# Optimization experiments

Hardware: AMD Instinct MI355X
Metric: run time of the kernel (lower is better)

The kernel has to match this reference:

```python
import jax, jax.numpy as jnp
import numpy as np

N = 100000   # nodes
E = 1600000  # edges per meta-path graph
D_IN = 256
H = 4        # num_heads
F = 32       # out_feats per head
D_HID = H * F  # 128
D_SEM = 128  # semantic attention hidden dim
C = 8        # output classes
NEG_SLOPE = 0.2


def setup_inputs() -> dict:
    key = jax.random.key(0)
    ks = jax.random.split(key, 24)
    inp = {
        "x": jax.random.normal(ks[0], (N, D_IN), dtype=jnp.float32),
        "src0": jax.random.randint(ks[1], (E,), 0, N),
        "dst0": jax.random.randint(ks[2], (E,), 0, N),
        "ew0": jax.random.uniform(ks[3], (E,), dtype=jnp.float32),
        "src1": jax.random.randint(ks[4], (E,), 0, N),
        "dst1": jax.random.randint(ks[5], (E,), 0, N),
        "ew1": jax.random.uniform(ks[6], (E,), dtype=jnp.float32),
    }
    s_in = 1.0 / np.sqrt(D_IN)
    s_f = 1.0 / np.sqrt(F)
    s_h = 1.0 / np.sqrt(D_HID)
    s_s = 1.0 / np.sqrt(D_SEM)
    # GAT params for meta-path 0 and 1 (tuple feat -> separate fc_src/fc_dst)
    inp["Wsrc0"] = jax.random.normal(ks[7], (D_IN, D_HID), dtype=jnp.float32) * s_in
    inp["Wdst0"] = jax.random.normal(ks[8], (D_IN, D_HID), dtype=jnp.float32) * s_in
    inp["al0"] = jax.random.normal(ks[9], (H, F), dtype=jnp.float32) * s_f
    inp["ar0"] = jax.random.normal(ks[10], (H, F), dtype=jnp.float32) * s_f
    inp["b0"] = jnp.zeros((D_HID,), dtype=jnp.float32)
    inp["Wsrc1"] = jax.random.normal(ks[11], (D_IN, D_HID), dtype=jnp.float32) * s_in
    inp["Wdst1"] = jax.random.normal(ks[12], (D_IN, D_HID), dtype=jnp.float32) * s_in
    inp["al1"] = jax.random.normal(ks[13], (H, F), dtype=jnp.float32) * s_f
    inp["ar1"] = jax.random.normal(ks[14], (H, F), dtype=jnp.float32) * s_f
    inp["b1"] = jnp.zeros((D_HID,), dtype=jnp.float32)
    # Semantic attention: Linear(D_HID->128) -> tanh -> Linear(128->1, no bias)
    inp["Wp1"] = jax.random.normal(ks[15], (D_HID, D_SEM), dtype=jnp.float32) * s_h
    inp["bp1"] = jnp.zeros((D_SEM,), dtype=jnp.float32)
    inp["Wp2"] = jax.random.normal(ks[16], (D_SEM, 1), dtype=jnp.float32) * s_s
    # Prediction head
    inp["Wo"] = jax.random.normal(ks[17], (D_HID, C), dtype=jnp.float32) * s_h
    inp["bo"] = jnp.zeros((C,), dtype=jnp.float32)
    return inp


def gat_conv(x, Wsrc, Wdst, al, ar, b, src, dst, ew):
    # feat_src/feat_dst: [N, H, F]
    fs = (x @ Wsrc).reshape(N, H, F)
    fd = (x @ Wdst).reshape(N, H, F)
    el = jnp.einsum('nhf,hf->nh', fs, al)  # [N, H]
    er = jnp.einsum('nhf,hf->nh', fd, ar)  # [N, H]
    e = jax.nn.leaky_relu(el[src] + er[dst], negative_slope=NEG_SLOPE)  # [E, H]
    a = jax.nn.sigmoid(e) * ew[:, None]  # [E, H]  (sigmoid attention * edge_weight)
    m = fs[src] * a[:, :, None]  # [E, H, F]
    out = jax.ops.segment_sum(m, dst, num_segments=N)  # [N, H, F]
    out = out + b.reshape(1, H, F)
    return jax.nn.elu(out).reshape(N, H * F)


def semantic_attention(z, Wp1, bp1, Wp2):
    # z: [N, P, D_HID]
    w = jnp.tanh(z @ Wp1 + bp1) @ Wp2  # [N, P, 1]
    w = w.mean(axis=0)                  # [P, 1]
    beta = jax.nn.softmax(w, axis=0)    # softmax over meta-paths
    return (beta[None] * z).sum(axis=1)  # [N, D_HID]


def reference(x, src0, dst0, ew0, src1, dst1, ew1,
              Wsrc0, Wdst0, al0, ar0, b0,
              Wsrc1, Wdst1, al1, ar1, b1,
              Wp1, bp1, Wp2, Wo, bo):
    z0 = gat_conv(x, Wsrc0, Wdst0, al0, ar0, b0, src0, dst0, ew0)
    z1 = gat_conv(x, Wsrc1, Wdst1, al1, ar1, b1, src1, dst1, ew1)
    z = jnp.stack([z0, z1], axis=1)  # [N, 2, H*F]
    h = semantic_attention(z, Wp1, bp1, Wp2)  # [N, H*F]
    return h @ Wo + bo  # [N, C]
```

## Files before the change

### kernel.cpp

```cpp
#include <hip/hip_runtime.h>
#include <hip/hip_fp16.h>
#include <math.h>

#define N_NODES 100000
#define N_EDGES 1600000
#define D_IN    256
#define D_HID   128
#define NH      4
#define NF      32
#define D_SEM   128
#define NC      8
#define NEG_SLOPE 0.2f
#define BUCKET  64
#define BIN_SHIFT 9
#define BINS    196
#define BIN_CAP 9216
#define CHUNK   8192

typedef _Float16 half8 __attribute__((ext_vector_type(8)));
typedef float    floatx4 __attribute__((ext_vector_type(4)));

struct BinArgs {
    const int*   src[2];
    const int*   dst[2];
    const float* ew[2];
    int*         gcur[2];
    uint2*       binned[2];
};
struct BucketArgs {
    const int*   gcur[2];
    const uint2* binned[2];
    int*         cnt[2];
    unsigned*    edg[2];
};

__global__ __launch_bounds__(256) void prep(const float* __restrict__ Ws0,
                                            const float* __restrict__ Ws1,
                                            const float* __restrict__ Wd0,
                                            const float* __restrict__ ar0,
                                            const float* __restrict__ Wd1,
                                            const float* __restrict__ ar1,
                                            const float* __restrict__ Wp1,
                                            __half* __restrict__ WTA,
                                            __half* __restrict__ WP1T) {
    int g = blockIdx.x * 256 + threadIdx.x;
    if (g < 32768) {
        int col = g >> 8, k = g & 255;
        WTA[(size_t)col*256 + k] = __float2half_rn(Ws0[k*D_HID + col]);
    } else if (g < 65536) {
        int g2 = g - 32768;
        int col = g2 >> 8, k = g2 & 255;
        WTA[(size_t)(128 + col)*256 + k] = __float2half_rn(Ws1[k*D_HID + col]);
    } else if (g < 73728) {
        int g2 = g - 65536;
        int j = g2 >> 8, k = g2 & 255;
        int p = j >> 4, hh = j & 15;
        float s = 0.f;
        if (hh < 4) {
            const float* Wd = p ? Wd1 : Wd0;
            const float* ar = p ? ar1 : ar0;
            for (int f = 0; f < NF; ++f)
                s = fmaf(Wd[k*D_HID + hh*NF + f], ar[hh*NF + f], s);
        }
        WTA[(size_t)(256 + j)*256 + k] = __float2half_rn(s);
    } else if (g < 90112) {
        int g2 = g - 73728;
        int c = g2 >> 7, k = g2 & 127;
        WP1T[g2] = __float2half_rn(Wp1[k*D_SEM + c]);
    }
}

__global__ __launch_bounds__(256, 4) void fs_half(const float* __restrict__ x,
                                                  const __half* __restrict__ WTA,
                                                  const float* __restrict__ al0,
                                                  const float* __restrict__ al1,
                                                  __half* __restrict__ FS0,
                                                  __half* __restrict__ FS1,
                                                  float* __restrict__ eler) {
    __shared__ unsigned short xs[64][256];
    __shared__ unsigned short wsB[144][64];
    int tid = threadIdx.x;
    int row0 = blockIdx.x * 64;
    int P = blockIdx.y;
    __half* FSP = P ? FS1 : FS0;
    int wid = tid >> 6, lane = tid & 63;
    int lr = lane & 15, lk = lane >> 4;

    #pragma unroll
    for (int i = 0; i < 8; ++i) {
        int id = tid + i*256;
        int r = id >> 5, c8 = (id & 31) << 3;
        int grow = row0 + r;
        float4 v0 = make_float4(0.f,0.f,0.f,0.f), v1 = v0;
        if (grow < N_NODES) {
            v0 = *(const float4*)&x[(size_t)grow*D_IN + c8];
            v1 = *(const float4*)&x[(size_t)grow*D_IN + c8 + 4];
        }
        __half2 h0 = __floats2half2_rn(v0.x, v0.y);
        __half2 h1 = __floats2half2_rn(v0.z, v0.w);
        __half2 h2 = __floats2half2_rn(v1.x, v1.y);
        __half2 h3 = __floats2half2_rn(v1.z, v1.w);
        uint4 pk;
        pk.x = *(unsigned*)&h0; pk.y = *(unsigned*)&h1;
        pk.z = *(unsigned*)&h2; pk.w = *(unsigned*)&h3;
        int ch = c8 >> 3;
        *(uint4*)&xs[r][((ch ^ (r & 7)) << 3)] = pk;
    }

    floatx4 acc[4][2];
    floatx4 acc4[4];
    #pragma unroll
    for (int m = 0; m < 4; ++m) {
        acc4[m] = (floatx4){0.f, 0.f, 0.f, 0.f};
        #pragma unroll
        for (int n = 0; n < 2; ++n) acc[m][n] = (floatx4){0.f, 0.f, 0.f, 0.f};
    }
    __syncthreads();

    for (int kc = 0; kc < 4; ++kc) {
        #pragma unroll
        for (int i = 0; i < 9; ++i) {
            int id = tid + i*256;
            int cl = id >> 4, c4 = (id & 15) << 2;
            int gcol = (cl < 128) ? (P*128 + cl) : (256 + P*16 + (cl - 128));
            uint2 pk = *(const uint2*)&WTA[(size_t)gcol*256 + kc*64 + c4];
            int cc = (((c4 >> 3) ^ (cl & 7)) << 3) + (c4 & 7);
            *(uint2*)&wsB[cl][cc] = pk;
        }
        __syncthreads();
        #pragma unroll
        for (int kk = 0; kk < 2; ++kk) {
            int kl = kk*4 + lk;
            int kg = kc*8 + kl;
            half8 a[4], b[2], b4;
            #pragma unroll
            for (int n = 0; n < 2; ++n) {
                int cl = wid*32 + n*16 + lr;
                b[n] = *(half8*)&wsB[cl][((kl ^ (cl & 7)) << 3)];
            }
            if (wid == 0) {
                int cl = 128 + lr;
                b4 = *(half8*)&wsB[cl][((kl ^ (cl & 7)) << 3)];
            }
            #pragma unroll
            for (int m = 0; m < 4; ++m) {
                int r = m*16 + lr;
                a[m] = *(half8*)&xs[r][((kg ^ (r & 7)) << 3)];
            }
            #pragma unroll
            for (int m = 0; m < 4; ++m)
                #pragma unroll
                for (int n = 0; n < 2; ++n)
                    acc[m][n] = __builtin_amdgcn_mfma_f32_16x16x32_f16(a[m], b[n], acc[m][n], 0, 0, 0);
            if (wid == 0) {
                #pragma unroll
                for (int m = 0; m < 4; ++m)
                    acc4[m] = __builtin_amdgcn_mfma_f32_16x16x32_f16(a[m], b4, acc4[m], 0, 0, 0);
            }
        }
        __syncthreads();
    }

    {
        const float* al = P ? al1 : al0;
        float av0 = al[wid*NF + lr];
        float av1 = al[wid*NF + 16 + lr];
        #pragma unroll
        for (int m = 0; m < 4; ++m)
            #pragma unroll
            for (int r4 = 0; r4 < 4; ++r4) {
                float s0 = acc[m][0][r4]*av0 + acc[m][1][r4]*av1;
                #pragma unroll
                for (int o = 1; o < 16; o <<= 1) s0 += __shfl_xor(s0, o);
                int row = row0 + m*16 + lk*4 + r4;
                if (lr == 0 && row < N_NODES)
                    eler[(P*2)*400000 + row*4 + wid] = s0;
            }
    }
    if (wid == 0 && lr < 4) {
        #pragma unroll
        for (int m = 0; m < 4; ++m)
            #pragma unroll
            for (int r4 = 0; r4 < 4; ++r4) {
                int row = row0 + m*16 + lk*4 + r4;
                if (row < N_NODES)
                    eler[(P*2+1)*400000 + row*4 + lr] = acc4[m][r4];
            }
    }

    __syncthreads();
    unsigned short* cstage = &xs[0][0];
    #pragma unroll
    for (int n = 0; n < 2; ++n) {
        int cl = wid*32 + n*16 + lr;
        #pragma unroll
        for (int m = 0; m < 4; ++m)
            #pragma unroll
            for (int r4 = 0; r4 < 4; ++r4) {
                int rr = m*16 + lk*4 + r4;
                __half hv = __float2half_rn(acc[m][n][r4]);
                cstage[rr*128 + cl] = *(unsigned short*)&hv;
            }
    }
    __syncthreads();
    #pragma unroll
    for (int i = 0; i < 4; ++i) {
        int id = tid + i*256;
        int r = id >> 4, c8 = (id & 15) << 3;
        int grow = row0 + r;
        if (grow < N_NODES)
            *(uint4*)&FSP[(size_t)grow*D_HID + c8] = *(uint4*)&cstage[r*128 + c8];
    }
}

__global__ __launch_bounds__(1024) void bin_kernel(BinArgs A) {
    __shared__ uint2 stage[CHUNK];
    __shared__ unsigned char binof[CHUNK];
    __shared__ int bcnt[256], boff[256], gbase[256], brun[256];
    int P = blockIdx.y;
    const int*   src = A.src[P];
    const int*   dst = A.dst[P];
    const float* ew  = A.ew[P];
    int*         gcur = A.gcur[P];
    uint2*       binned = A.binned[P];

    int tid = threadIdx.x;
    int c0 = blockIdx.x * CHUNK;
    int C = N_EDGES - c0; if (C > CHUNK) C = CHUNK;
    if (C <= 0) return;

    if (tid < 256) bcnt[tid] = 0;
    __syncthreads();
    for (int j = tid; j < C; j += 1024)
        atomicAdd(&bcnt[dst[c0 + j] >> BIN_SHIFT], 1);
    __syncthreads();

    int v = (tid < 256) ? bcnt[tid] : 0;
    if (tid < 256) boff[tid] = v;
    __syncthreads();
    for (int o = 1; o < 256; o <<= 1) {
        int u = (tid < 256 && tid >= o) ? boff[tid - o] : 0;
        __syncthreads();
        if (tid < 256) boff[tid] += u;
        __syncthreads();
    }
    if (tid < 256) {
        boff[tid] -= v;
        brun[tid] = 0;
        if (tid < BINS) gbase[tid] = v ? atomicAdd(&gcur[tid], v) : 0;
    }
    __syncthreads();

    for (int j = tid; j < C; j += 1024) {
        int e = c0 + j;
        int d = dst[e];
        int b = d >> BIN_SHIFT;
        unsigned q = (unsigned)(ew[e] * 32767.f + 0.5f);
        int p = atomicAdd(&brun[b], 1);
        int sl = boff[b] + p;
        stage[sl] = make_uint2(((unsigned)src[e] << 15) | q, (unsigned)d);
        binof[sl] = (unsigned char)b;
    }
    __syncthreads();

    for (int j = tid; j < C; j += 1024) {
        int b = binof[j];
        int off = gbase[b] + (j - boff[b]);
        if (off < BIN_CAP) binned[b * BIN_CAP + off] = stage[j];
    }
}

__global__ __launch_bounds__(1024) void bucket_kernel(BucketArgs A) {
    __shared__ unsigned buck[256 * BUCKET];
    __shared__ int lcnt[256];
    int P = blockIdx.y;
    const int*   gcur   = A.gcur[P];
    const uint2* binned = A.binned[P];
    int*         cnt    = A.cnt[P];
    unsigned*    edg    = A.edg[P];

    int tid = threadIdx.x;
    int nb = blockIdx.x;
    int b  = nb >> 1;
    int n0 = nb << 8;
    int lo = (nb & 1) << 8;
    if (tid < 256) lcnt[tid] = 0;
    __syncthreads();

    int cE = gcur[b]; if (cE > BIN_CAP) cE = BIN_CAP;
    int bn0 = b << BIN_SHIFT;
    for (int j = tid; j < cE; j += 1024) {
        uint2 r = binned[b * BIN_CAP + j];
        int w = ((int)r.y - bn0) - lo;
        if ((unsigned)w < 256u) {
            int p = atomicAdd(&lcnt[w], 1);
            if (p < BUCKET) buck[(w << 6) + p] = r.x;
        }
    }
    __syncthreads();

    const uint4* b4 = (const uint4*)buck;
    uint4* e4 = (uint4*)edg;
    for (int i = tid; i < 256 * BUCKET / 4; i += 1024) {
        int node = n0 + (i >> 4);
        int used = lcnt[i >> 4];
        if (node < N_NODES && ((i & 15) << 2) < used)
            e4[((size_t)node << 4) + (i & 15)] = b4[i];
    }
    if (tid < 256) {
        int node = n0 + tid;
        if (node < N_NODES) cnt[node] = lcnt[tid] < BUCKET ? lcnt[tid] : BUCKET;
    }
}

__global__ __launch_bounds__(256) void agg_kernel(const __half* __restrict__ FS,
                                                  const float* __restrict__ el,
                                                  const float* __restrict__ er,
                                                  const int* __restrict__ cnt,
                                                  const unsigned* __restrict__ edg,
                                                  const float* __restrict__ bias,
                                                  __half* __restrict__ zh) {
    int wv = (blockIdx.x * 256 + threadIdx.x) >> 6;
    int lane = threadIdx.x & 63;
    if (wv >= N_NODES) return;
    int q  = lane >> 4;
    int ql = lane & 15;
    int hh = lane & 3;
    float erh = er[wv*4 + hh];
    int cn = cnt[wv];
    if (cn > BUCKET) cn = BUCKET;
    int beg = wv << 6;
    const __half* fsq = FS + (ql << 3);

    float4 a0 = make_float4(0.f,0.f,0.f,0.f);
    float4 a1 = make_float4(0.f,0.f,0.f,0.f);

    int nIt = (cn + 15) >> 4;
    for (int it = 0; it < nIt; ++it) {
        int jb = it << 4;
        int sl = jb + (lane >> 2);
        int slc = sl < cn ? sl : cn - 1;
        unsigned w = edg[beg + slc];
        int s = (int)(w >> 15);
        float a = (float)(w & 32767u) * (1.f / 32767.f);
        float v = el[s*4 + hh] + erh;
        v = v > 0.f ? v : NEG_SLOPE * v;
        a = a * __builtin_amdgcn_rcpf(1.f + __expf(-v));
        a = sl < cn ? a : 0.f;
        #pragma unroll
        for (int u = 0; u < 4; ++u) {
            int e = (u << 2) + q;
            int su = jb + e;
            int ssrc = __shfl(s, e << 2);
            uint4 raw = make_uint4(0u, 0u, 0u, 0u);
            if (su < cn) raw = *(const uint4*)&fsq[(size_t)ssrc * D_HID];
            float av = __shfl(a, (e << 2) | (ql >> 2));
            float2 f0 = __half22float2(*(__half2*)&raw.x);
            float2 f1 = __half22float2(*(__half2*)&raw.y);
            float2 f2 = __half22float2(*(__half2*)&raw.z);
            float2 f3 = __half22float2(*(__half2*)&raw.w);
            a0.x = fmaf(f0.x, av, a0.x); a0.y = fmaf(f0.y, av, a0.y);
            a0.z = fmaf(f1.x, av, a0.z); a0.w = fmaf(f1.y, av, a0.w);
            a1.x = fmaf(f2.x, av, a1.x); a1.y = fmaf(f2.y, av, a1.y);
            a1.z = fmaf(f3.x, av, a1.z); a1.w = fmaf(f3.y, av, a1.w);
        }
    }

    #pragma unroll
    for (int o = 16; o < 64; o <<= 1) {
        a0.x += __shfl_xor(a0.x, o); a0.y += __shfl_xor(a0.y, o);
        a0.z += __shfl_xor(a0.z, o); a0.w += __shfl_xor(a0.w, o);
        a1.x += __shfl_xor(a1.x, o); a1.y += __shfl_xor(a1.y, o);
        a1.z += __shfl_xor(a1.z, o); a1.w += __shfl_xor(a1.w, o);
    }

    if (q < 2) {
        int c = (ql << 3) + (q << 2);
        float4 r = q ? a1 : a0;
        float4 bv = *(const float4*)&bias[c];
        r.x += bv.x; r.y += bv.y; r.z += bv.z; r.w += bv.w;
        r.x = r.x > 0.f ? r.x : expm1f(r.x);
        r.y = r.y > 0.f ? r.y : expm1f(r.y);
        r.z = r.z > 0.f ? r.z : expm1f(r.z);
        r.w = r.w > 0.f ? r.w : expm1f(r.w);
        __half2 h0 = __floats2half2_rn(r.x, r.y);
        __half2 h1 = __floats2half2_rn(r.z, r.w);
        uint2 pk; pk.x = *(unsigned*)&h0; pk.y = *(unsigned*)&h1;
        *(uint2*)&zh[(size_t)wv*D_HID + c] = pk;
    }
}

__global__ __launch_bounds__(256) void sem_mfma(const __half* __restrict__ zh0,
                                                const __half* __restrict__ zh1,
                                                const __half* __restrict__ WP1T,
                                                const float* __restrict__ bp1,
                                                const float* __restrict__ Wp2,
                                                float* __restrict__ wsum) {
    __shared__ unsigned short zs[64][128];
    __shared__ unsigned short ps[128][128];
    __shared__ float red[4];
    const __half* z = blockIdx.y ? zh1 : zh0;
    int tid = threadIdx.x;
    int row0 = blockIdx.x * 64;
    int wid = tid >> 6, lane = tid & 63;
    int wm = wid >> 1, wn = wid & 1;
    int lr = lane & 15, lk = lane >> 4;

    #pragma unroll
    for (int i = 0; i < 4; ++i) {
        int id = tid + i*256;
        int r = id >> 4, ch = id & 15;
        int grow = row0 + r;
        uint4 pk = make_uint4(0u, 0u, 0u, 0u);
        if (grow < N_NODES) pk = *(const uint4*)&z[(size_t)grow*D_HID + (ch << 3)];
        *(uint4*)&zs[r][((ch ^ (r & 7)) << 3)] = pk;
    }
    #pragma unroll
    for (int i = 0; i < 16; ++i) {
        int id = tid + i*256;
        int c = id >> 5, k4 = (id & 31) << 2;
        uint2 pk = *(const uint2*)&WP1T[c*128 + k4];
        int cc = (((k4 >> 3) ^ (c & 7)) << 3) + (k4 & 7);
        *(uint2*)&ps[c][cc] = pk;
    }
    __syncthreads();

    floatx4 acc[2][4];
    #pragma unroll
    for (int m = 0; m < 2; ++m)
        #pragma unroll
        for (int n = 0; n < 4; ++n) acc[m][n] = (floatx4){0.f, 0.f, 0.f, 0.f};

    #pragma unroll
    for (int kk = 0; kk < 4; ++kk) {
        int ksub = kk*4 + lk;
        half8 a[2], b[4];
        #pragma unroll
        for (int m = 0; m < 2; ++m) {
            int r = wm*32 + m*16 + lr;
            a[m] = *(half8*)&zs[r][((ksub ^ (r & 7)) << 3)];
        }
        #pragma unroll
        for (int n = 0; n < 4; ++n) {
            int c = wn*64 + n*16 + lr;
            b[n] = *(half8*)&ps[c][((ksub ^ (c & 7)) << 3)];
        }
        #pragma unroll
        for (int m = 0; m < 2; ++m)
            #pragma unroll
            for (int n = 0; n < 4; ++n)
                acc[m][n] = __builtin_amdgcn_mfma_f32_16x16x32_f16(a[m], b[n], acc[m][n], 0, 0, 0);
    }

    float s = 0.f;
    #pragma unroll
    for (int m = 0; m < 2; ++m)
        #pragma unroll
        for (int n = 0; n < 4; ++n) {
            int col = wn*64 + n*16 + lr;
            float bp = bp1[col];
            float w2 = Wp2[col];
            #pragma unroll
            for (int r4 = 0; r4 < 4; ++r4) {
                int grow = row0 + wm*32 + m*16 + lk*4 + r4;
                if (grow < N_NODES) {
                    float v = acc[m][n][r4] + bp;
                    float t = 1.f - 2.f / (__expf(2.f*v) + 1.f);
                    s = fmaf(t, w2, s);
                }
            }
        }
    #pragma unroll
    for (int o = 1; o < 64; o <<= 1) s += __shfl_xor(s, o);
    if (lane == 0) red[wid] = s;
    __syncthreads();
    if (tid == 0) atomicAdd(&wsum[blockIdx.y], red[0] + red[1] + red[2] + red[3]);
}

__global__ __launch_bounds__(256) void final_kernel(const __half* __restrict__ zh0,
                                                    const __half* __restrict__ zh1,
                                                    const float* __restrict__ Wo,
                                                    const float* __restrict__ bo,
                                                    const float* __restrict__ wsum,
                                                    float* __restrict__ out) {
    __shared__ float z0s[32][132];
    __shared__ float z1s[32][132];
    __shared__ float wos[128*8];
    __shared__ float bos[8];
    int tid = threadIdx.x;
    int n0 = blockIdx.x * 32;
    #pragma unroll
    for (int i = 0; i < 4; ++i) wos[tid + i*256] = Wo[tid + i*256];
    if (tid < 8) bos[tid] = bo[tid];
    #pragma unroll
    for (int i = 0; i < 2; ++i) {
        int id = tid + i*256;
        int r = id >> 4, c8 = (id & 15) << 3;
        uint4 p0 = *(const uint4*)&zh0[(size_t)(n0 + r)*D_HID + c8];
        uint4 p1 = *(const uint4*)&zh1[(size_t)(n0 + r)*D_HID + c8];
        float2 q0 = __half22float2(*(__half2*)&p0.x);
        float2 q1 = __half22float2(*(__half2*)&p0.y);
        float2 q2 = __half22float2(*(__half2*)&p0.z);
        float2 q3 = __half22float2(*(__half2*)&p0.w);
        *(float4*)&z0s[r][c8]     = make_float4(q0.x, q0.y, q1.x, q1.y);
        *(float4*)&z0s[r][c8 + 4] = make_float4(q2.x, q2.y, q3.x, q3.y);
        q0 = __half22float2(*(__half2*)&p1.x);
        q1 = __half22float2(*(__half2*)&p1.y);
        q2 = __half22float2(*(__half2*)&p1.z);
        q3 = __half22float2(*(__half2*)&p1.w);
        *(float4*)&z1s[r][c8]     = make_float4(q0.x, q0.y, q1.x, q1.y);
        *(float4*)&z1s[r][c8 + 4] = make_float4(q2.x, q2.y, q3.x, q3.y);
    }
    __syncthreads();

    float w0 = wsum[0] * (1.f / N_NODES), w1 = wsum[1] * (1.f / N_NODES);
    float m = fmaxf(w0, w1);
    float e0 = __expf(w0 - m), e1 = __expf(w1 - m);
    float b0 = e0 / (e0 + e1), b1 = 1.f - b0;

    int node = tid >> 3, c = tid & 7;
    float s = bos[c];
    #pragma unroll 8
    for (int k = 0; k < 128; ++k) {
        float hk = b0 * z0s[node][k] + b1 * z1s[node][k];
        s = fmaf(hk, wos[k*8 + c], s);
    }
    out[(n0 + node)*NC + c] = s;
}

extern "C" void kernel_launch(void* const* d_in, const int* in_sizes, int n_in,
                              void* d_out, int out_size, void* d_ws, size_t ws_size,
                              hipStream_t stream) {
    const float* x     = (const float*)d_in[0];
    const int*   src0  = (const int*)  d_in[1];
    const int*   dst0  = (const int*)  d_in[2];
    const float* ew0   = (const float*)d_in[3];
    const int*   src1  = (const int*)  d_in[4];
    const int*   dst1  = (const int*)  d_in[5];
    const float* ew1   = (const float*)d_in[6];
    const float* Wsrc0 = (const float*)d_in[7];
    const float* Wdst0 = (const float*)d_in[8];
    const float* al0   = (const float*)d_in[9];
    const float* ar0   = (const float*)d_in[10];
    const float* b0    = (const float*)d_in[11];
    const float* Wsrc1 = (const float*)d_in[12];
    const float* Wdst1 = (const float*)d_in[13];
    const float* al1   = (const float*)d_in[14];
    const float* ar1   = (const float*)d_in[15];
    const float* b1    = (const float*)d_in[16];
    const float* Wp1   = (const float*)d_in[17];
    const float* bp1   = (const float*)d_in[18];
    const float* Wp2   = (const float*)d_in[19];
    const float* Wo    = (const float*)d_in[20];
    const float* bo    = (const float*)d_in[21];
    float* out = (float*)d_out;

    float*    ws     = (float*)d_ws;
    __half*   FS0    = (__half*)ws;
    __half*   FS1    = (__half*)(ws + 6400000);
    __half*   ZH0    = (__half*)(ws + 12800000);
    __half*   ZH1    = (__half*)(ws + 19200000);
    float*    ELER   = ws + 25600000;
    float*    WSUM   = ELER + 1600000;
    __half*   WTA    = (__half*)(WSUM + 8);
    __half*   WP1T   = (__half*)((float*)WTA + 36864);
    int*      CNT0   = (int*)((float*)WP1T + 8192);
    int*      CNT1   = CNT0  + 100000;
    int*      GCUR0  = CNT1  + 100000;
    int*      GCUR1  = GCUR0 + 256;
    unsigned* EDG0   = (unsigned*)(GCUR1 + 256);
    uint2*    BINNED0= (uint2*)(EDG0 + 6400000);
    float*    endser = (float*)BINNED0 + 2*(size_t)BINS*BIN_CAP;
    unsigned* EDG1   = (unsigned*)endser;
    uint2*    BINNED1= (uint2*)(EDG1 + 6400000);
    size_t fused_bytes = (size_t)((float*)BINNED1 + 2*(size_t)BINS*BIN_CAP - ws) * 4;
    bool fused = ws_size >= fused_bytes;
    if (!fused) { EDG1 = EDG0; BINNED1 = BINNED0; }

    hipMemsetAsync(GCUR0, 0, sizeof(int)*512, stream);
    hipMemsetAsync(WSUM, 0, sizeof(float)*4, stream);

    prep<<<352, 256, 0, stream>>>(Wsrc0, Wsrc1, Wdst0, ar0, Wdst1, ar1, Wp1, WTA, WP1T);
    dim3 fsgrid((N_NODES + 63)/64, 2);
    fs_half<<<fsgrid, 256, 0, stream>>>(x, WTA, al0, al1, FS0, FS1, ELER);

    int nchunks = (N_EDGES + CHUNK - 1) / CHUNK;
    if (fused) {
        BinArgs ba = {{src0, src1}, {dst0, dst1}, {ew0, ew1},
                      {GCUR0, GCUR1}, {BINNED0, BINNED1}};
        bin_kernel<<<dim3(nchunks, 2), 1024, 0, stream>>>(ba);
        BucketArgs ka = {{GCUR0, GCUR1}, {BINNED0, BINNED1},
                         {CNT0, CNT1}, {EDG0, EDG1}};
        bucket_kernel<<<dim3(2*BINS, 2), 1024, 0, stream>>>(ka);
        agg_kernel<<<(N_NODES*64)/256, 256, 0, stream>>>(FS0, ELER, ELER + 400000, CNT0, EDG0, b0, ZH0);
        agg_kernel<<<(N_NODES*64)/256, 256, 0, stream>>>(FS1, ELER + 800000, ELER + 1200000, CNT1, EDG1, b1, ZH1);
    } else {
        BinArgs ba0 = {{src0, src0}, {dst0, dst0}, {ew0, ew0},
                       {GCUR0, GCUR0}, {BINNED0, BINNED0}};
        BucketArgs ka0 = {{GCUR0, GCUR0}, {BINNED0, BINNED0},
                          {CNT0, CNT0}, {EDG0, EDG0}};
        bin_kernel<<<dim3(nchunks, 1), 1024, 0, stream>>>(ba0);
        bucket_kernel<<<dim3(2*BINS, 1), 1024, 0, stream>>>(ka0);
        agg_kernel<<<(N_NODES*64)/256, 256, 0, stream>>>(FS0, ELER, ELER + 400000, CNT0, EDG0, b0, ZH0);
        BinArgs ba1 = {{src1, src1}, {dst1, dst1}, {ew1, ew1},
                       {GCUR1, GCUR1}, {BINNED0, BINNED0}};
        BucketArgs ka1 = {{GCUR1, GCUR1}, {BINNED0, BINNED0},
                          {CNT1, CNT1}, {EDG0, EDG0}};
        bin_kernel<<<dim3(nchunks, 1), 1024, 0, stream>>>(ba1);
        bucket_kernel<<<dim3(2*BINS, 1), 1024, 0, stream>>>(ka1);
        agg_kernel<<<(N_NODES*64)/256, 256, 0, stream>>>(FS1, ELER + 800000, ELER + 1200000, CNT1, EDG0, b1, ZH1);
    }

    dim3 semgrid((N_NODES + 63)/64, 2);
    sem_mfma<<<semgrid, 256, 0, stream>>>(ZH0, ZH1, WP1T, bp1, Wp2, WSUM);
    final_kernel<<<N_NODES/32, 256, 0, stream>>>(ZH0, ZH1, Wo, bo, WSUM, out);
}
```

Baseline: 521.5 us.

## Fuse bucketing and GAT aggregation into one kernel using LDS-resident edge buckets

Merges the bucket and aggregation kernels so each 1024-thread block builds per-node edge buckets in shared memory and immediately aggregates them, with each wave handling 16 nodes in sequence. This removes the global EDG/CNT round trip and two kernel launches. In exchange, occupancy drops because of the 64KB LDS per block, and each wave now processes nodes serially, which may expose gather latency. Only 784 blocks run the aggregation instead of the previous large grid.

```diff
diff --git a/kernel.cpp b/kernel.cpp
--- a/kernel.cpp
+++ b/kernel.cpp
@@ -27,11 +27,14 @@
     int*         gcur[2];
     uint2*       binned[2];
 };
-struct BucketArgs {
-    const int*   gcur[2];
-    const uint2* binned[2];
-    int*         cnt[2];
-    unsigned*    edg[2];
+struct BAArgs {
+    const int*    gcur[2];
+    const uint2*  binned[2];
+    const __half* fs[2];
+    const float*  el[2];
+    const float*  er[2];
+    const float*  bias[2];
+    __half*       zh[2];
 };
 
 __global__ __launch_bounds__(256) void prep(const float* __restrict__ Ws0,
@@ -270,14 +273,17 @@
     }
 }
 
-__global__ __launch_bounds__(1024) void bucket_kernel(BucketArgs A) {
+__global__ __launch_bounds__(1024) void bucket_agg(BAArgs A) {
     __shared__ unsigned buck[256 * BUCKET];
     __shared__ int lcnt[256];
     int P = blockIdx.y;
-    const int*   gcur   = A.gcur[P];
-    const uint2* binned = A.binned[P];
-    int*         cnt    = A.cnt[P];
-    unsigned*    edg    = A.edg[P];
+    const int*    gcur   = A.gcur[P];
+    const uint2*  binned = A.binned[P];
+    const __half* FS     = A.fs[P];
+    const float*  el     = A.el[P];
+    const float*  er     = A.er[P];
+    const float*  bias   = A.bias[P];
+    __half*       zh     = A.zh[P];
 
     int tid = threadIdx.x;
     int nb = blockIdx.x;
@@ -299,94 +305,77 @@
     }
     __syncthreads();
 
-    const uint4* b4 = (const uint4*)buck;
-    uint4* e4 = (uint4*)edg;
-    for (int i = tid; i < 256 * BUCKET / 4; i += 1024) {
-        int node = n0 + (i >> 4);
-        int used = lcnt[i >> 4];
-        if (node < N_NODES && ((i & 15) << 2) < used)
-            e4[((size_t)node << 4) + (i & 15)] = b4[i];
-    }
-    if (tid < 256) {
-        int node = n0 + tid;
-        if (node < N_NODES) cnt[node] = lcnt[tid] < BUCKET ? lcnt[tid] : BUCKET;
-    }
-}
-
-__global__ __launch_bounds__(256) void agg_kernel(const __half* __restrict__ FS,
-                                                  const float* __restrict__ el,
-                                                  const float* __restrict__ er,
-                                                  const int* __restrict__ cnt,
-                                                  const unsigned* __restrict__ edg,
-                                                  const float* __restrict__ bias,
-                                                  __half* __restrict__ zh) {
-    int wv = (blockIdx.x * 256 + threadIdx.x) >> 6;
-    int lane = threadIdx.x & 63;
-    if (wv >= N_NODES) return;
+    int wvid = tid >> 6, lane = tid & 63;
     int q  = lane >> 4;
     int ql = lane & 15;
     int hh = lane & 3;
-    float erh = er[wv*4 + hh];
-    int cn = cnt[wv];
-    if (cn > BUCKET) cn = BUCKET;
-    int beg = wv << 6;
     const __half* fsq = FS + (ql << 3);
 
-    float4 a0 = make_float4(0.f,0.f,0.f,0.f);
-    float4 a1 = make_float4(0.f,0.f,0.f,0.f);
-
-    int nIt = (cn + 15) >> 4;
-    for (int it = 0; it < nIt; ++it) {
-        int jb = it << 4;
-        int sl = jb + (lane >> 2);
-        int slc = sl < cn ? sl : cn - 1;
-        unsigned w = edg[beg + slc];
-        int s = (int)(w >> 15);
-        float a = (float)(w & 32767u) * (1.f / 32767.f);
-        float v = el[s*4 + hh] + erh;
-        v = v > 0.f ? v : NEG_SLOPE * v;
-        a = a * __builtin_amdgcn_rcpf(1.f + __expf(-v));
-        a = sl < cn ? a : 0.f;
-        #pragma unroll
-        for (int u = 0; u < 4; ++u) {
-            int e = (u << 2) + q;
-            int su = jb + e;
-            int ssrc = __shfl(s, e << 2);
-            uint4 raw = make_uint4(0u, 0u, 0u, 0u);
-            if (su < cn) raw = *(const uint4*)&fsq[(size_t)ssrc * D_HID];
-            float av = __shfl(a, (e << 2) | (ql >> 2));
-            float2 f0 = __half22float2(*(__half2*)&raw.x);
-            float2 f1 = __half22float2(*(__half2*)&raw.y);
-            float2 f2 = __half22float2(*(__half2*)&raw.z);
-            float2 f3 = __half22float2(*(__half2*)&raw.w);
-            a0.x = fmaf(f0.x, av, a0.x); a0.y = fmaf(f0.y, av, a0.y);
-            a0.z = fmaf(f1.x, av, a0.z); a0.w = fmaf(f1.y, av, a0.w);
-            a1.x = fmaf(f2.x, av, a1.x); a1.y = fmaf(f2.y, av, a1.y);
-            a1.z = fmaf(f3.x, av, a1.z); a1.w = fmaf(f3.y, av, a1.w);
-        }
-    }
-
-    #pragma unroll
-    for (int o = 16; o < 64; o <<= 1) {
-        a0.x += __shfl_xor(a0.x, o); a0.y += __shfl_xor(a0.y, o);
-        a0.z += __shfl_xor(a0.z, o); a0.w += __shfl_xor(a0.w, o);
-        a1.x += __shfl_xor(a1.x, o); a1.y += __shfl_xor(a1.y, o);
-        a1.z += __shfl_xor(a1.z, o); a1.w += __shfl_xor(a1.w, o);
-    }
-
-    if (q < 2) {
-        int c = (ql << 3) + (q << 2);
-        float4 r = q ? a1 : a0;
-        float4 bv = *(const float4*)&bias[c];
-        r.x += bv.x; r.y += bv.y; r.z += bv.z; r.w += bv.w;
-        r.x = r.x > 0.f ? r.x : expm1f(r.x);
-        r.y = r.y > 0.f ? r.y : expm1f(r.y);
-        r.z = r.z > 0.f ? r.z : expm1f(r.z);
-        r.w = r.w > 0.f ? r.w : expm1f(r.w);
-        __half2 h0 = __floats2half2_rn(r.x, r.y);
-        __half2 h1 = __floats2half2_rn(r.z, r.w);
-        uint2 pk; pk.x = *(unsigned*)&h0; pk.y = *(unsigned*)&h1;
-        *(uint2*)&zh[(size_t)wv*D_HID + c] = pk;
+    for (int t = 0; t < 16; ++t) {
+        int nl = wvid*16 + t;
+        int node = n0 + nl;
+        if (node >= N_NODES) break;
+        int cn = lcnt[nl];
+        if (cn > BUCKET) cn = BUCKET;
+        float erh = er[node*4 + hh];
+        unsigned* bk = &buck[nl << 6];
+
+        float4 a0 = make_float4(0.f,0.f,0.f,0.f);
+        float4 a1 = make_float4(0.f,0.f,0.f,0.f);
+
+        int nIt = (cn + 15) >> 4;
+        for (int it = 0; it < nIt; ++it) {
+            int jb = it << 4;
+            int sl = jb + (lane >> 2);
+            int slc = sl < cn ? sl : cn - 1;
+            unsigned w = bk[slc];
+            int s = (int)(w >> 15);
+            float a = (float)(w & 32767u) * (1.f / 32767.f);
+            float v = el[s*4 + hh] + erh;
+            v = v > 0.f ? v : NEG_SLOPE * v;
+            a = a * __builtin_amdgcn_rcpf(1.f + __expf(-v));
+            a = sl < cn ? a : 0.f;
+            #pragma unroll
+            for (int u = 0; u < 4; ++u) {
+                int e = (u << 2) + q;
+                int su = jb + e;
+                int ssrc = __shfl(s, e << 2);
+                uint4 raw = make_uint4(0u, 0u, 0u, 0u);
+                if (su < cn) raw = *(const uint4*)&fsq[(size_t)ssrc * D_HID];
+                float av = __shfl(a, (e << 2) | (ql >> 2));
+                float2 f0 = __half22float2(*(__half2*)&raw.x);
+                float2 f1 = __half22float2(*(__half2*)&raw.y);
+                float2 f2 = __half22float2(*(__half2*)&raw.z);
+                float2 f3 = __half22float2(*(__half2*)&raw.w);
+                a0.x = fmaf(f0.x, av, a0.x); a0.y = fmaf(f0.y, av, a0.y);
+                a0.z = fmaf(f1.x, av, a0.z); a0.w = fmaf(f1.y, av, a0.w);
+                a1.x = fmaf(f2.x, av, a1.x); a1.y = fmaf(f2.y, av, a1.y);
+                a1.z = fmaf(f3.x, av, a1.z); a1.w = fmaf(f3.y, av, a1.w);
+            }
+        }
+
+        #pragma unroll
+        for (int o = 16; o < 64; o <<= 1) {
+            a0.x += __shfl_xor(a0.x, o); a0.y += __shfl_xor(a0.y, o);
+            a0.z += __shfl_xor(a0.z, o); a0.w += __shfl_xor(a0.w, o);
+            a1.x += __shfl_xor(a1.x, o); a1.y += __shfl_xor(a1.y, o);
+            a1.z += __shfl_xor(a1.z, o); a1.w += __shfl_xor(a1.w, o);
+        }
+
+        if (q < 2) {
+            int c = (ql << 3) + (q << 2);
+            float4 r = q ? a1 : a0;
+            float4 bv = *(const float4*)&bias[c];
+            r.x += bv.x; r.y += bv.y; r.z += bv.z; r.w += bv.w;
+            r.x = r.x > 0.f ? r.x : expm1f(r.x);
+            r.y = r.y > 0.f ? r.y : expm1f(r.y);
+            r.z = r.z > 0.f ? r.z : expm1f(r.z);
+            r.w = r.w > 0.f ? r.w : expm1f(r.w);
+            __half2 h0 = __floats2half2_rn(r.x, r.y);
+            __half2 h1 = __floats2half2_rn(r.z, r.w);
+            uint2 pk; pk.x = *(unsigned*)&h0; pk.y = *(unsigned*)&h1;
+            *(uint2*)&zh[(size_t)node*D_HID + c] = pk;
+        }
     }
 }
 
@@ -564,18 +553,14 @@
     float*    WSUM   = ELER + 1600000;
     __half*   WTA    = (__half*)(WSUM + 8);
     __half*   WP1T   = (__half*)((float*)WTA + 36864);
-    int*      CNT0   = (int*)((float*)WP1T + 8192);
-    int*      CNT1   = CNT0  + 100000;
-    int*      GCUR0  = CNT1  + 100000;
+    int*      GCUR0  = (int*)((float*)WP1T + 8192);
     int*      GCUR1  = GCUR0 + 256;
-    unsigned* EDG0   = (unsigned*)(GCUR1 + 256);
-    uint2*    BINNED0= (uint2*)(EDG0 + 6400000);
+    uint2*    BINNED0= (uint2*)(GCUR1 + 256);
     float*    endser = (float*)BINNED0 + 2*(size_t)BINS*BIN_CAP;
-    unsigned* EDG1   = (unsigned*)endser;
-    uint2*    BINNED1= (uint2*)(EDG1 + 6400000);
+    uint2*    BINNED1= (uint2*)endser;
     size_t fused_bytes = (size_t)((float*)BINNED1 + 2*(size_t)BINS*BIN_CAP - ws) * 4;
     bool fused = ws_size >= fused_bytes;
-    if (!fused) { EDG1 = EDG0; BINNED1 = BINNED0; }
+    if (!fused) BINNED1 = BINNED0;
 
     hipMemsetAsync(GCUR0, 0, sizeof(int)*512, stream);
     hipMemsetAsync(WSUM, 0, sizeof(float)*4, stream);
@@ -585,30 +570,33 @@
     fs_half<<<fsgrid, 256, 0, stream>>>(x, WTA, al0, al1, FS0, FS1, ELER);
 
     int nchunks = (N_EDGES + CHUNK - 1) / CHUNK;
+    const float* EL0 = ELER;
+    const float* ER0 = ELER + 400000;
+    const float* EL1 = ELER + 800000;
+    const float* ER1 = ELER + 1200000;
     if (fused) {
         BinArgs ba = {{src0, src1}, {dst0, dst1}, {ew0, ew1},
                       {GCUR0, GCUR1}, {BINNED0, BINNED1}};
         bin_kernel<<<dim3(nchunks, 2), 1024, 0, stream>>>(ba);
-        BucketArgs ka = {{GCUR0, GCUR1}, {BINNED0, BINNED1},
-                         {CNT0, CNT1}, {EDG0, EDG1}};
-        bucket_kernel<<<dim3(2*BINS, 2), 1024, 0, stream>>>(ka);
-        agg_kernel<<<(N_NODES*64)/256, 256, 0, stream>>>(FS0, ELER, ELER + 400000, CNT0, EDG0, b0, ZH0);
-        agg_kernel<<<(N_NODES*64)/256, 256, 0, stream>>>(FS1, ELER + 800000, ELER + 1200000, CNT1, EDG1, b1, ZH1);
+        BAArgs ka = {{GCUR0, GCUR1}, {BINNED0, BINNED1},
+                     {(const __half*)FS0, (const __half*)FS1},
+                     {EL0, EL1}, {ER0, ER1}, {b0, b1}, {ZH0, ZH1}};
+        bucket_agg<<<dim3(2*BINS, 2), 1024, 0, stream>>>(ka);
     } else {
         BinArgs ba0 = {{src0, src0}, {dst0, dst0}, {ew0, ew0},
                        {GCUR0, GCUR0}, {BINNED0, BINNED0}};
-        BucketArgs ka0 = {{GCUR0, GCUR0}, {BINNED0, BINNED0},
-                          {CNT0, CNT0}, {EDG0, EDG0}};
         bin_kernel<<<dim3(nchunks, 1), 1024, 0, stream>>>(ba0);
-        bucket_kernel<<<dim3(2*BINS, 1), 1024, 0, stream>>>(ka0);
-        agg_kernel<<<(N_NODES*64)/256, 256, 0, stream>>>(FS0, ELER, ELER + 400000, CNT0, EDG0, b0, ZH0);
+        BAArgs ka0 = {{GCUR0, GCUR0}, {BINNED0, BINNED0},
+                      {(const __half*)FS0, (const __half*)FS0},
+                      {EL0, EL0}, {ER0, ER0}, {b0, b0}, {ZH0, ZH0}};
+        bucket_agg<<<dim3(2*BINS, 1), 1024, 0, stream>>>(ka0);
         BinArgs ba1 = {{src1, src1}, {dst1, dst1}, {ew1, ew1},
                        {GCUR1, GCUR1}, {BINNED0, BINNED0}};
-        BucketArgs ka1 = {{GCUR1, GCUR1}, {BINNED0, BINNED0},
-                          {CNT1, CNT1}, {EDG0, EDG0}};
         bin_kernel<<<dim3(nchunks, 1), 1024, 0, stream>>>(ba1);
-        bucket_kernel<<<dim3(2*BINS, 1), 1024, 0, stream>>>(ka1);
-        agg_kernel<<<(N_NODES*64)/256, 256, 0, stream>>>(FS1, ELER + 800000, ELER + 1200000, CNT1, EDG0, b1, ZH1);
+        BAArgs ka1 = {{GCUR1, GCUR1}, {BINNED0, BINNED0},
+                      {(const __half*)FS1, (const __half*)FS1},
+                      {EL1, EL1}, {ER1, ER1}, {b1, b1}, {ZH1, ZH1}};
+        bucket_agg<<<dim3(2*BINS, 1), 1024, 0, stream>>>(ka1);
     }
 
     dim3 semgrid((N_NODES + 63)/64, 2);
```

Result: no change. 527.6 us (+1.2%).
